# Optimization experiments

Measured on AMD Instinct MI355X. Metric: run time of the kernel, lower is better.

Reference implementation:

```python
import jax, jax.numpy as jnp
import numpy as np

D_MODEL = 1024
EXPAND = 2
D_INNER = EXPAND * D_MODEL          # 2048
D_STATE = 64
NGROUPS = 1
HEADDIM = 128
NHEADS = D_INNER // HEADDIM         # 16
D_CONV = 4
CONV_DIM = D_INNER + 2 * NGROUPS * D_STATE      # 2176
D_IN_PROJ = 2 * D_INNER + 2 * NGROUPS * D_STATE + NHEADS  # 4240
BATCH = 2
SEQLEN = 4096
RMS_EPS = 1e-5


def setup_inputs() -> dict:
    key = jax.random.key(0)
    ks = jax.random.split(key, 8)
    u = jax.random.normal(ks[0], (BATCH, SEQLEN, D_MODEL), jnp.float32)
    in_proj_w = jax.random.normal(ks[1], (D_IN_PROJ, D_MODEL), jnp.float32) * 0.02
    conv_w = jax.random.normal(ks[2], (CONV_DIM, D_CONV), jnp.float32) * 0.2
    conv_b = jax.random.normal(ks[3], (CONV_DIM,), jnp.float32) * 0.1
    dt_bias = jax.random.normal(ks[4], (NHEADS,), jnp.float32) * 0.5
    # A ~ Uniform(1,16), A_log = log(A)  (as in Mamba2 init)
    A_log = jnp.log(jax.random.uniform(ks[5], (NHEADS,), jnp.float32, 1.0, 16.0))
    D = jnp.ones((NHEADS,), jnp.float32)
    rms_w = jnp.ones((D_INNER,), jnp.float32)
    out_w = jax.random.normal(ks[6], (D_MODEL, D_INNER), jnp.float32) * 0.02
    return {"u": u, "in_proj_w": in_proj_w, "conv_w": conv_w, "conv_b": conv_b,
            "dt_bias": dt_bias, "A_log": A_log, "D": D, "rms_w": rms_w, "out_w": out_w}


def reference(u, in_proj_w, conv_w, conv_b, dt_bias, A_log, D, rms_w, out_w):
    Bsz, L, _ = u.shape
    # in_proj: (B,L,d_model) -> (B,L,d_in_proj), split [z, x, B, C, dt]
    zxbcdt = jnp.einsum('bld,ed->ble', u, in_proj_w)
    s1 = D_INNER
    s2 = 2 * D_INNER
    s3 = s2 + NGROUPS * D_STATE
    s4 = s3 + NGROUPS * D_STATE
    z = zxbcdt[..., :s1]
    x = zxbcdt[..., s1:s2]
    B_part = zxbcdt[..., s2:s3]
    C_part = zxbcdt[..., s3:s4]
    dt = zxbcdt[..., s4:]
    dt = jax.nn.softplus(dt + dt_bias)            # (B,L,H), dt_limit=(0,inf) -> no clamp

    # depthwise causal conv1d + silu over [x, B, C]
    xBC = jnp.concatenate([x, B_part, C_part], axis=-1)      # (B,L,CONV_DIM)
    xt = xBC.transpose(0, 2, 1)                              # (B,C,L)
    kern = conv_w[:, None, :]                                # (C,1,W)
    conv = jax.lax.conv_general_dilated(
        xt, kern, (1,), [(D_CONV - 1, 0)],
        dimension_numbers=('NCH', 'OIH', 'NCH'),
        feature_group_count=CONV_DIM)
    xBC = jax.nn.silu((conv + conv_b[None, :, None]).transpose(0, 2, 1))

    x_c = xBC[..., :D_INNER]
    B_c = xBC[..., D_INNER:D_INNER + NGROUPS * D_STATE]
    C_c = xBC[..., D_INNER + NGROUPS * D_STATE:]
    x_s = x_c.reshape(Bsz, L, NHEADS, HEADDIM)               # (B,L,H,P)
    hpg = NHEADS // NGROUPS
    B_full = jnp.repeat(B_c.reshape(Bsz, L, NGROUPS, D_STATE), hpg, axis=2)  # (B,L,H,N)
    C_full = jnp.repeat(C_c.reshape(Bsz, L, NGROUPS, D_STATE), hpg, axis=2)

    A = -jnp.exp(A_log)                                      # (H,)

    def step(state, inp):
        x_t, dt_t, B_t, C_t = inp  # (B,H,P),(B,H),(B,H,N),(B,H,N)
        decay = jnp.exp(dt_t * A)[:, :, None, None]          # (B,H,1,1)
        state = decay * state + B_t[:, :, None, :] * x_t[..., None]  # (B,H,P,N)
        y_t = jnp.einsum('bhpn,bhn->bhp', state, C_t)
        return state, y_t

    init = jnp.zeros((Bsz, NHEADS, HEADDIM, D_STATE), u.dtype)
    xs = (x_s.transpose(1, 0, 2, 3), dt.transpose(1, 0, 2),
          B_full.transpose(1, 0, 2, 3), C_full.transpose(1, 0, 2, 3))
    _, ys = jax.lax.scan(step, init, xs)                     # (L,B,H,P)
    y = ys.transpose(1, 0, 2, 3) + D[None, None, :, None] * x_s

    y_flat = y.reshape(Bsz, L, D_INNER)
    mu = jnp.mean(y_flat * y_flat, axis=-1, keepdims=True)
    y_flat = y_flat * jax.lax.rsqrt(mu + RMS_EPS) * rms_w    # RMSNorm
    y_flat = y_flat * jax.nn.sigmoid(z)                      # gate
    return jnp.einsum('bld,ed->ble', y_flat, out_w)          # out_proj (no bias)
```

## Files before the change

### kernel.cpp

```cpp
#include <hip/hip_runtime.h>
#include <math.h>

#define D_MODEL   1024
#define D_INNER   2048
#define D_STATE   64
#define HEADDIM   128
#define NHEADS    16
#define D_CONV    4
#define BATCH     2
#define SEQLEN    4096
#define RMS_EPS   1e-5f
#define D_IN_PROJ 4240

#define ZX_LD     4224

#define LCHUNK    128
#define NCHUNK    (SEQLEN / LCHUNK)

typedef __attribute__((ext_vector_type(8))) short short8;
typedef __attribute__((ext_vector_type(4))) float f32x4;

__device__ __forceinline__ ushort f2bf(float f) {
  unsigned u = __float_as_uint(f);
  u += 0x7fff + ((u >> 16) & 1);
  return (ushort)(u >> 16);
}
__device__ __forceinline__ float bf2f(ushort h) {
  return __uint_as_float(((unsigned)h) << 16);
}
__device__ __forceinline__ void ld4(const float* p, float* d) {
  float4 v = *(const float4*)p; d[0] = v.x; d[1] = v.y; d[2] = v.z; d[3] = v.w;
}
__device__ __forceinline__ void ld4b(const ushort* p, float* d) {
  ushort4 v = *(const ushort4*)p;
  d[0] = bf2f(v.x); d[1] = bf2f(v.y); d[2] = bf2f(v.z); d[3] = bf2f(v.w);
}

__device__ __forceinline__ void gl_lds16(const ushort* g, ushort* l) {
  __builtin_amdgcn_global_load_lds(
      (const __attribute__((address_space(1))) unsigned int*)g,
      (__attribute__((address_space(3))) unsigned int*)l, 16, 0, 0);
}

__global__ void cvt_split(const float* __restrict__ w,
                          ushort* __restrict__ hi, ushort* __restrict__ lo, int n4) {
  int i = blockIdx.x * 256 + threadIdx.x;
  if (i >= n4) return;
  float4 v = ((const float4*)w)[i];
  ushort h0 = f2bf(v.x), h1 = f2bf(v.y), h2 = f2bf(v.z), h3 = f2bf(v.w);
  ushort l0 = f2bf(v.x - bf2f(h0)), l1 = f2bf(v.y - bf2f(h1));
  ushort l2 = f2bf(v.z - bf2f(h2)), l3 = f2bf(v.w - bf2f(h3));
  ((ushort4*)hi)[i] = make_ushort4(h0, h1, h2, h3);
  ((ushort4*)lo)[i] = make_ushort4(l0, l1, l2, l3);
}

template<int BM, int BK, bool ALO, bool OBF16>
__launch_bounds__(256, 3)
__global__ void gemm_bf16p(const ushort* __restrict__ Ah, const ushort* __restrict__ Al,
                           const ushort* __restrict__ Bh, const ushort* __restrict__ Bl,
                           float* __restrict__ C, int ldc,
                           int M, int N, int ldab, int Kslice, int n1term) {
  constexpr int BN = 128;
  constexpr int NQ = BK / 8;
  constexpr int RT = BM / 32;
  constexpr int CT = 4;
  constexpr int KS = BK / 32;

  __shared__ ushort As[ALO ? 2 : 1][BM * BK];
  __shared__ ushort Bs[2][BN * BK];

  const int bn   = blockIdx.x * BN;
  if (bn >= N) return;
  const bool two = (bn >= n1term);
  const int t    = threadIdx.x;
  const int bm   = blockIdx.y * BM;
  const int kz   = blockIdx.z;
  const int kb   = kz * Kslice;
  C += (size_t)kz * M * ldc;
  const int wave = t >> 6, lane = t & 63;
  const int ml   = lane & 15, g4 = lane >> 4;
  const int sw   = ml & (NQ - 1);
  const int wr   = wave & 1, wc = wave >> 1;
  const int r0   = wr * RT * 16, c0 = wc * CT * 16;

  f32x4 acc[RT][CT];
#pragma unroll
  for (int i = 0; i < RT; ++i)
#pragma unroll
    for (int j = 0; j < CT; ++j) acc[i][j] = (f32x4){0.f, 0.f, 0.f, 0.f};

  for (int k0 = kb; k0 < kb + Kslice; k0 += BK) {
    __syncthreads();
#pragma unroll
    for (int ii = 0; ii < BM * NQ / 256; ++ii) {
      int idx = t + ii * 256;
      int row = idx / NQ, qs = idx % NQ;
      int qg  = qs ^ (row & (NQ - 1));
      size_t go = (size_t)(bm + row) * ldab + k0 + qg * 8;
      gl_lds16(Ah + go, &As[0][idx * 8]);
      if (ALO) gl_lds16(Al + go, &As[ALO ? 1 : 0][idx * 8]);
    }
#pragma unroll
    for (int ii = 0; ii < BN * NQ / 256; ++ii) {
      int idx = t + ii * 256;
      int row = idx / NQ, qs = idx % NQ;
      int qg  = qs ^ (row & (NQ - 1));
      size_t go = (size_t)(bn + row) * ldab + k0 + qg * 8;
      gl_lds16(Bh + go, &Bs[0][idx * 8]);
      if (two) gl_lds16(Bl + go, &Bs[1][idx * 8]);
    }
    __syncthreads();

#pragma unroll
    for (int ks = 0; ks < KS; ++ks) {
      const int qA = ((ks * 4 + g4) ^ sw) * 8;
      short8 ah[RT], al[RT], bh[CT], bl[CT];
#pragma unroll
      for (int i = 0; i < RT; ++i) {
        int off = (r0 + i * 16 + ml) * BK + qA;
        ah[i] = *(const short8*)&As[0][off];
        if (ALO) al[i] = *(const short8*)&As[ALO ? 1 : 0][off];
      }
#pragma unroll
      for (int j = 0; j < CT; ++j) {
        int off = (c0 + j * 16 + ml) * BK + qA;
        bh[j] = *(const short8*)&Bs[0][off];
        if (two) bl[j] = *(const short8*)&Bs[1][off];
      }
#pragma unroll
      for (int i = 0; i < RT; ++i)
#pragma unroll
        for (int j = 0; j < CT; ++j) {
          acc[i][j] = __builtin_amdgcn_mfma_f32_16x16x32_bf16(ah[i], bh[j], acc[i][j], 0, 0, 0);
          if (two)
            acc[i][j] = __builtin_amdgcn_mfma_f32_16x16x32_bf16(ah[i], bl[j], acc[i][j], 0, 0, 0);
          if (ALO)
            acc[i][j] = __builtin_amdgcn_mfma_f32_16x16x32_bf16(al[i], bh[j], acc[i][j], 0, 0, 0);
        }
    }
  }

#pragma unroll
  for (int i = 0; i < RT; ++i)
#pragma unroll
    for (int j = 0; j < CT; ++j) {
      int col = bn + c0 + j * 16 + ml;
      if (col < N) {
        int rowb = bm + r0 + i * 16 + g4 * 4;
#pragma unroll
        for (int r = 0; r < 4; ++r) {
          if (OBF16) ((ushort*)C)[(size_t)(rowb + r) * ldc + col] = f2bf(acc[i][j][r]);
          else       C[(size_t)(rowb + r) * ldc + col] = acc[i][j][r];
        }
      }
    }
}

__global__ void add_out(const float* __restrict__ P, float* __restrict__ out, int n4) {
  int i = blockIdx.x * 256 + threadIdx.x;
  if (i >= n4) return;
  float4 a = ((const float4*)P)[i];
  float4 b = ((const float4*)(P + (size_t)SEQLEN * D_MODEL))[i];
  ((float4*)out)[i] = make_float4(a.x + b.x, a.y + b.y, a.z + b.z, a.w + b.w);
}

__global__ void add_dt(const float* __restrict__ P, float* __restrict__ dtb) {
  int i = blockIdx.x * 256 + threadIdx.x;
  if (i >= SEQLEN * NHEADS / 4) return;
  float4 s = ((const float4*)P)[i];
#pragma unroll
  for (int k = 1; k < 8; ++k) {
    float4 v = ((const float4*)(P + (size_t)k * SEQLEN * NHEADS))[i];
    s.x += v.x; s.y += v.y; s.z += v.z; s.w += v.w;
  }
  ((float4*)dtb)[i] = s;
}


__device__ __forceinline__ void cum_scan(float* cum, float v, int t, float* carry) {
  int lane = t & 63;
#pragma unroll
  for (int off = 1; off < 64; off <<= 1) {
    float o = __shfl_up(v, off);
    if (lane >= off) v += o;
  }
  if (t == 63) *carry = v;
  __syncthreads();
  if (t >= 64 && t < LCHUNK) v += *carry;
  if (t < LCHUNK) cum[t] = v;
  __syncthreads();
}

__device__ __forceinline__ void conv4b(const ushort* __restrict__ zx,
                                       const float* __restrict__ cw,
                                       const float* __restrict__ cb,
                                       int l, int col0, float* outv) {
  const ushort* bp = zx + (size_t)l * ZX_LD + col0;
  float r3[4], r2[4], r1[4], r0[4], bb[4];
  ld4b(bp, r3);
  if (l >= 1) ld4b(bp - ZX_LD, r2);     else { r2[0]=r2[1]=r2[2]=r2[3]=0.f; }
  if (l >= 2) ld4b(bp - 2 * ZX_LD, r1); else { r1[0]=r1[1]=r1[2]=r1[3]=0.f; }
  if (l >= 3) ld4b(bp - 3 * ZX_LD, r0); else { r0[0]=r0[1]=r0[2]=r0[3]=0.f; }
  const int ch = col0 - 2048;
  ld4(cb + ch, bb);
#pragma unroll
  for (int j = 0; j < 4; ++j) {
    float w4[4]; ld4(cw + (ch + j) * 4, w4);
    float a = bb[j];
    a = fmaf(w4[0], r0[j], a);
    a = fmaf(w4[1], r1[j], a);
    a = fmaf(w4[2], r2[j], a);
    a = fmaf(w4[3], r3[j], a);
    outv[j] = a / (1.f + __expf(-a));
  }
}

__launch_bounds__(256, 2)
__global__ void passA_ssd(const ushort* __restrict__ zx,
                          const float* __restrict__ dtb,
                          const float* __restrict__ cw, const float* __restrict__ cb,
                          const float* __restrict__ dt_bias,
                          const float* __restrict__ A_log,
                          float* __restrict__ Sc, float* __restrict__ Pc) {
  const int blk = blockIdx.x;
  const int c   = blk & (NCHUNK - 1);
  const int h   = blk >> 5;
  const int l0  = c * LCHUNK;
  const int t   = threadIdx.x;
  const int wave = t >> 6, lane = t & 63;
  const int ml = lane & 15, g4 = lane >> 4;
  const float Ah = -expf(A_log[h]);

  __shared__ float cum[LCHUNK];
  __shared__ float carry;
  __shared__ ushort Xt[2][LCHUNK * 40];
  __shared__ ushort Bt[2][D_STATE * 40];

  {
    float v = 0.f;
    if (t < LCHUNK) {
      float xv = dtb[(size_t)(l0 + t) * NHEADS + h] + dt_bias[h];
      float sp = (xv > 20.f) ? xv : log1pf(expf(xv));
      v = sp * Ah;
    }
    cum_scan(cum, v, t, &carry);
  }
  const float cend = cum[LCHUNK - 1];

  f32x4 acc[2][4];
#pragma unroll
  for (int i = 0; i < 2; ++i)
#pragma unroll
    for (int j = 0; j < 4; ++j) acc[i][j] = (f32x4){0.f, 0.f, 0.f, 0.f};
  const int p0 = wave * 32;

  for (int slab = 0; slab < 4; ++slab) {
    __syncthreads();
    for (int i = 0; i < 4; ++i) {
      int q = t + i * 256;
      int s = q >> 5, p4 = (q & 31) * 4;
      int l = l0 + slab * 32 + s;
      float xv[4];
      conv4b(zx, cw, cb, l, 2048 + h * HEADDIM + p4, xv);
#pragma unroll
      for (int j = 0; j < 4; ++j) {
        ushort hh = f2bf(xv[j]);
        Xt[0][(p4 + j) * 40 + s] = hh;
        Xt[1][(p4 + j) * 40 + s] = f2bf(xv[j] - bf2f(hh));
      }
    }
    for (int i = 0; i < 2; ++i) {
      int q = t + i * 256;
      int s = q >> 4, n4 = (q & 15) * 4;
      int l = l0 + slab * 32 + s;
      float wd = __expf(cend - cum[slab * 32 + s]);
      float bv[4];
      conv4b(zx, cw, cb, l, 4096 + n4, bv);
#pragma unroll
      for (int j = 0; j < 4; ++j) {
        float val = bv[j] * wd;
        ushort hh = f2bf(val);
        Bt[0][(n4 + j) * 40 + s] = hh;
        Bt[1][(n4 + j) * 40 + s] = f2bf(val - bf2f(hh));
      }
    }
    __syncthreads();

    short8 xa_h[2], xa_l[2];
#pragma unroll
    for (int pi = 0; pi < 2; ++pi) {
      int off = (p0 + pi * 16 + ml) * 40 + g4 * 8;
      xa_h[pi] = *(const short8*)&Xt[0][off];
      xa_l[pi] = *(const short8*)&Xt[1][off];
    }
#pragma unroll
    for (int ni = 0; ni < 4; ++ni) {
      int off = (ni * 16 + ml) * 40 + g4 * 8;
      short8 bh = *(const short8*)&Bt[0][off];
      short8 bl = *(const short8*)&Bt[1][off];
#pragma unroll
      for (int pi = 0; pi < 2; ++pi) {
        acc[pi][ni] = __builtin_amdgcn_mfma_f32_16x16x32_bf16(xa_h[pi], bh, acc[pi][ni], 0, 0, 0);
        acc[pi][ni] = __builtin_amdgcn_mfma_f32_16x16x32_bf16(xa_h[pi], bl, acc[pi][ni], 0, 0, 0);
        acc[pi][ni] = __builtin_amdgcn_mfma_f32_16x16x32_bf16(xa_l[pi], bh, acc[pi][ni], 0, 0, 0);
      }
    }
  }

  float* S = Sc + (size_t)blk * (HEADDIM * D_STATE);
#pragma unroll
  for (int pi = 0; pi < 2; ++pi)
#pragma unroll
    for (int ni = 0; ni < 4; ++ni) {
      int n = ni * 16 + ml;
#pragma unroll
      for (int r = 0; r < 4; ++r) {
        int p = p0 + pi * 16 + g4 * 4 + r;
        S[(size_t)p * D_STATE + n] = acc[pi][ni][r];
      }
    }
  if (t == 0) Pc[blk] = __expf(cend);
}

__global__ void scan_passB(float* __restrict__ Sc, const float* __restrict__ Pc) {
  const int h = blockIdx.x;
  const int e = blockIdx.y * 512 + threadIdx.x;
  const size_t hb = (size_t)h * NCHUNK;
  float st = 0.f;
  for (int c = 0; c < NCHUNK; ++c) {
    size_t idx = (hb + c) * (HEADDIM * D_STATE) + e;
    float P = Pc[hb + c];
    float v = Sc[idx];
    Sc[idx] = st;
    st = fmaf(P, st, v);
  }
}

__launch_bounds__(256, 2)
__global__ void passC_ssd(const ushort* __restrict__ zx,
                          const float* __restrict__ dtb,
                          const float* __restrict__ cw, const float* __restrict__ cb,
                          const float* __restrict__ dt_bias,
                          const float* __restrict__ A_log,
                          const float* __restrict__ Dp,
                          const float* __restrict__ Sc,
                          float* __restrict__ ybuf) {
  const int blk = blockIdx.x;
  const int c   = blk & (NCHUNK - 1);
  const int h   = blk >> 5;
  const int l0  = c * LCHUNK;
  const int t   = threadIdx.x;
  const int wave = t >> 6, lane = t & 63;
  const int ml = lane & 15, g4 = lane >> 4;
  const float Ah = -expf(A_log[h]);
  const float Dh = Dp[h];

  __shared__ float cum[LCHUNK];
  __shared__ float carry;
  __shared__ ushort Csl[2][2][LCHUNK * 32];
  __shared__ ushort Bsl[2][2][32 * 32];
  __shared__ ushort Msl[2][LCHUNK * 32];
  __shared__ ushort Xt[2][LCHUNK * 40];

  {
    float v = 0.f;
    if (t < LCHUNK) {
      float xv = dtb[(size_t)(l0 + t) * NHEADS + h] + dt_bias[h];
      float sp = (xv > 20.f) ? xv : log1pf(expf(xv));
      v = sp * Ah;
    }
    cum_scan(cum, v, t, &carry);
  }

  {
    int row = t >> 1, half = t & 1;
    int l = l0 + row;
    int colbase = 4160 + half * 32;
#pragma unroll
    for (int j0 = 0; j0 < 32; j0 += 4) {
      float cv[4];
      conv4b(zx, cw, cb, l, colbase + j0, cv);
      ushort h0 = f2bf(cv[0]), h1 = f2bf(cv[1]), h2 = f2bf(cv[2]), h3 = f2bf(cv[3]);
      *(ushort4*)&Csl[half][0][row * 32 + j0] = make_ushort4(h0, h1, h2, h3);
      *(ushort4*)&Csl[half][1][row * 32 + j0] =
          make_ushort4(f2bf(cv[0] - bf2f(h0)), f2bf(cv[1] - bf2f(h1)),
                       f2bf(cv[2] - bf2f(h2)), f2bf(cv[3] - bf2f(h3)));
    }
  }

  f32x4 accY[2][8];
#pragma unroll
  for (int i = 0; i < 2; ++i)
#pragma unroll
    for (int j = 0; j < 8; ++j) accY[i][j] = (f32x4){0.f, 0.f, 0.f, 0.f};
  const int t0 = wave * 32;

  for (int slab = 0; slab < 4; ++slab) {
    __syncthreads();
    for (int i = 0; i < 2; ++i) {
      int q = t + i * 256;
      int s = q >> 4, c4 = (q & 15) * 4;
      int l = l0 + slab * 32 + s;
      float bv[4];
      conv4b(zx, cw, cb, l, 4096 + c4, bv);
      int ks = c4 >> 5, jj = c4 & 31;
      ushort h0 = f2bf(bv[0]), h1 = f2bf(bv[1]), h2 = f2bf(bv[2]), h3 = f2bf(bv[3]);
      *(ushort4*)&Bsl[ks][0][s * 32 + jj] = make_ushort4(h0, h1, h2, h3);
      *(ushort4*)&Bsl[ks][1][s * 32 + jj] =
          make_ushort4(f2bf(bv[0] - bf2f(h0)), f2bf(bv[1] - bf2f(h1)),
                       f2bf(bv[2] - bf2f(h2)), f2bf(bv[3] - bf2f(h3)));
    }
    for (int i = 0; i < 4; ++i) {
      int q = t + i * 256;
      int s = q >> 5, p4 = (q & 31) * 4;
      int l = l0 + slab * 32 + s;
      float xv[4];
      conv4b(zx, cw, cb, l, 2048 + h * HEADDIM + p4, xv);
#pragma unroll
      for (int j = 0; j < 4; ++j) {
        ushort hh = f2bf(xv[j]);
        Xt[0][(p4 + j) * 40 + s] = hh;
        Xt[1][(p4 + j) * 40 + s] = f2bf(xv[j] - bf2f(hh));
      }
    }
    __syncthreads();

    f32x4 g[2][2];
#pragma unroll
    for (int i = 0; i < 2; ++i)
#pragma unroll
      for (int j = 0; j < 2; ++j) g[i][j] = (f32x4){0.f, 0.f, 0.f, 0.f};
#pragma unroll
    for (int ks = 0; ks < 2; ++ks) {
      short8 ca_h[2], ca_l[2];
#pragma unroll
      for (int ti = 0; ti < 2; ++ti) {
        int off = (t0 + ti * 16 + ml) * 32 + g4 * 8;
        ca_h[ti] = *(const short8*)&Csl[ks][0][off];
        ca_l[ti] = *(const short8*)&Csl[ks][1][off];
      }
#pragma unroll
      for (int si = 0; si < 2; ++si) {
        int off = (si * 16 + ml) * 32 + g4 * 8;
        short8 bh = *(const short8*)&Bsl[ks][0][off];
        short8 bl = *(const short8*)&Bsl[ks][1][off];
#pragma unroll
        for (int ti = 0; ti < 2; ++ti) {
          g[ti][si] = __builtin_amdgcn_mfma_f32_16x16x32_bf16(ca_h[ti], bh, g[ti][si], 0, 0, 0);
          g[ti][si] = __builtin_amdgcn_mfma_f32_16x16x32_bf16(ca_h[ti], bl, g[ti][si], 0, 0, 0);
          g[ti][si] = __builtin_amdgcn_mfma_f32_16x16x32_bf16(ca_l[ti], bh, g[ti][si], 0, 0, 0);
        }
      }
    }
#pragma unroll
    for (int ti = 0; ti < 2; ++ti)
#pragma unroll
      for (int si = 0; si < 2; ++si) {
        int sl = si * 16 + ml;
        int sg = slab * 32 + sl;
#pragma unroll
        for (int r = 0; r < 4; ++r) {
          int tg = t0 + ti * 16 + g4 * 4 + r;
          float coeff = (sg <= tg) ? __expf(cum[tg] - cum[sg]) : 0.f;
          float val = g[ti][si][r] * coeff + ((sg == tg) ? Dh : 0.f);
          ushort hh = f2bf(val);
          Msl[0][tg * 32 + sl] = hh;
          Msl[1][tg * 32 + sl] = f2bf(val - bf2f(hh));
        }
      }
    __syncthreads();
    {
      short8 ma_h[2], ma_l[2];
#pragma unroll
      for (int ti = 0; ti < 2; ++ti) {
        int off = (t0 + ti * 16 + ml) * 32 + g4 * 8;
        ma_h[ti] = *(const short8*)&Msl[0][off];
        ma_l[ti] = *(const short8*)&Msl[1][off];
      }
#pragma unroll
      for (int pi = 0; pi < 8; ++pi) {
        int off = (pi * 16 + ml) * 40 + g4 * 8;
        short8 xh = *(const short8*)&Xt[0][off];
        short8 xl = *(const short8*)&Xt[1][off];
#pragma unroll
        for (int ti = 0; ti < 2; ++ti) {
          accY[ti][pi] = __builtin_amdgcn_mfma_f32_16x16x32_bf16(ma_h[ti], xh, accY[ti][pi], 0, 0, 0);
          accY[ti][pi] = __builtin_amdgcn_mfma_f32_16x16x32_bf16(ma_h[ti], xl, accY[ti][pi], 0, 0, 0);
          accY[ti][pi] = __builtin_amdgcn_mfma_f32_16x16x32_bf16(ma_l[ti], xh, accY[ti][pi], 0, 0, 0);
        }
      }
    }
  }

  const float* S = Sc + (size_t)blk * (HEADDIM * D_STATE);
  for (int ns = 0; ns < 2; ++ns) {
    __syncthreads();
    for (int i = 0; i < 4; ++i) {
      int q = t + i * 256;
      int p = q >> 3, j4 = (q & 7) * 4;
      float4 v = *(const float4*)(S + (size_t)p * D_STATE + ns * 32 + j4);
      float vv[4] = {v.x, v.y, v.z, v.w};
      ushort hh0 = f2bf(vv[0]), hh1 = f2bf(vv[1]), hh2 = f2bf(vv[2]), hh3 = f2bf(vv[3]);
      *(ushort4*)&Xt[0][p * 40 + j4] = make_ushort4(hh0, hh1, hh2, hh3);
      *(ushort4*)&Xt[1][p * 40 + j4] =
          make_ushort4(f2bf(vv[0] - bf2f(hh0)), f2bf(vv[1] - bf2f(hh1)),
                       f2bf(vv[2] - bf2f(hh2)), f2bf(vv[3] - bf2f(hh3)));
    }
    {
      int row = t >> 1, j0 = (t & 1) * 16;
      float e = __expf(cum[row]);
#pragma unroll
      for (int j = 0; j < 16; ++j) {
        int idx = row * 32 + j0 + j;
        float cv = bf2f(Csl[ns][0][idx]) + bf2f(Csl[ns][1][idx]);
        float val = cv * e;
        ushort hh = f2bf(val);
        Msl[0][idx] = hh;
        Msl[1][idx] = f2bf(val - bf2f(hh));
      }
    }
    __syncthreads();
    {
      short8 ma_h[2], ma_l[2];
#pragma unroll
      for (int ti = 0; ti < 2; ++ti) {
        int off = (t0 + ti * 16 + ml) * 32 + g4 * 8;
        ma_h[ti] = *(const short8*)&Msl[0][off];
        ma_l[ti] = *(const short8*)&Msl[1][off];
      }
#pragma unroll
      for (int pi = 0; pi < 8; ++pi) {
        int off = (pi * 16 + ml) * 40 + g4 * 8;
        short8 xh = *(const short8*)&Xt[0][off];
        short8 xl = *(const short8*)&Xt[1][off];
#pragma unroll
        for (int ti = 0; ti < 2; ++ti) {
          accY[ti][pi] = __builtin_amdgcn_mfma_f32_16x16x32_bf16(ma_h[ti], xh, accY[ti][pi], 0, 0, 0);
          accY[ti][pi] = __builtin_amdgcn_mfma_f32_16x16x32_bf16(ma_h[ti], xl, accY[ti][pi], 0, 0, 0);
          accY[ti][pi] = __builtin_amdgcn_mfma_f32_16x16x32_bf16(ma_l[ti], xh, accY[ti][pi], 0, 0, 0);
        }
      }
    }
  }

#pragma unroll
  for (int ti = 0; ti < 2; ++ti)
#pragma unroll
    for (int pi = 0; pi < 8; ++pi) {
      int p = pi * 16 + ml;
#pragma unroll
      for (int r = 0; r < 4; ++r) {
        int l = l0 + t0 + ti * 16 + g4 * 4 + r;
        ybuf[(size_t)l * D_INNER + h * HEADDIM + p] = accY[ti][pi][r];
      }
    }
}

__launch_bounds__(256)
__global__ void rmsnorm_gate_split(const float* __restrict__ ybuf,
                                   const ushort* __restrict__ zx,
                                   const float* __restrict__ rms_w,
                                   ushort* __restrict__ yh) {
  const int row = blockIdx.x;
  const int t   = threadIdx.x;
  const float* y  = ybuf + (size_t)row * D_INNER;
  const ushort* z = zx   + (size_t)row * ZX_LD;

  float4 a  = *(const float4*)(y + t * 8);
  float4 bq = *(const float4*)(y + t * 8 + 4);
  float ss = a.x * a.x + a.y * a.y + a.z * a.z + a.w * a.w +
             bq.x * bq.x + bq.y * bq.y + bq.z * bq.z + bq.w * bq.w;
#pragma unroll
  for (int off = 32; off > 0; off >>= 1) ss += __shfl_down(ss, off);
  __shared__ float red[4];
  if ((t & 63) == 0) red[t >> 6] = ss;
  __syncthreads();
  float tot = red[0] + red[1] + red[2] + red[3];
  float scale = rsqrtf(tot * (1.f / (float)D_INNER) + RMS_EPS);

  float vy[8] = {a.x, a.y, a.z, a.w, bq.x, bq.y, bq.z, bq.w};
  ushort4 zv0 = *(const ushort4*)(z + t * 8);
  ushort4 zv1 = *(const ushort4*)(z + t * 8 + 4);
  ushort zz[8] = {zv0.x, zv0.y, zv0.z, zv0.w, zv1.x, zv1.y, zv1.z, zv1.w};
  ushort hh[8];
#pragma unroll
  for (int jj = 0; jj < 8; ++jj) {
    int col = t * 8 + jj;
    float g = 1.f / (1.f + __expf(-bf2f(zz[jj])));
    float v = vy[jj] * scale * rms_w[col] * g;
    hh[jj] = f2bf(v);
  }
  size_t o = (size_t)row * D_INNER + t * 8;
  *(ushort4*)(yh + o)     = make_ushort4(hh[0], hh[1], hh[2], hh[3]);
  *(ushort4*)(yh + o + 4) = make_ushort4(hh[4], hh[5], hh[6], hh[7]);
}

extern "C" void kernel_launch(void* const* d_in, const int* in_sizes, int n_in,
                              void* d_out, int out_size, void* d_ws, size_t ws_size,
                              hipStream_t stream) {
  const float* u         = (const float*)d_in[0];
  const float* in_proj_w = (const float*)d_in[1];
  const float* conv_w    = (const float*)d_in[2];
  const float* conv_b    = (const float*)d_in[3];
  const float* dt_bias   = (const float*)d_in[4];
  const float* A_log     = (const float*)d_in[5];
  const float* Dp        = (const float*)d_in[6];
  const float* rms_w     = (const float*)d_in[7];
  const float* out_w     = (const float*)d_in[8];
  float* out = (float*)d_out;

  float* ws    = (float*)d_ws;
  ushort* zxbc = (ushort*)ws;
  float* dtb   = ws   + (size_t)SEQLEN * ZX_LD / 2;
  float* dtp   = dtb  + (size_t)SEQLEN * NHEADS;
  float* ybuf  = dtp  + (size_t)8 * SEQLEN * NHEADS;
  float* Pc    = ybuf + (size_t)SEQLEN * D_INNER;
  float* Sc    = Pc   + 512;
  ushort* uh   = (ushort*)(Sc + (size_t)NHEADS * NCHUNK * HEADDIM * D_STATE);
  ushort* ul   = uh  + (size_t)SEQLEN * D_MODEL;
  ushort* w1h  = ul  + (size_t)SEQLEN * D_MODEL;
  ushort* w1l  = w1h + (size_t)D_IN_PROJ * D_MODEL;
  ushort* w2h  = w1l + (size_t)D_IN_PROJ * D_MODEL;
  ushort* w2l  = w2h + (size_t)D_MODEL * D_INNER;
  ushort* yh   = (ushort*)Sc;
  float* Opart = ybuf;

  {
    int n4 = D_IN_PROJ * D_MODEL / 4;
    cvt_split<<<(n4 + 255) / 256, 256, 0, stream>>>(in_proj_w, w1h, w1l, n4);
    int m4 = D_MODEL * D_INNER / 4;
    cvt_split<<<(m4 + 255) / 256, 256, 0, stream>>>(out_w, w2h, w2l, m4);
  }

  for (int b = 0; b < BATCH; ++b) {
    const float* u_b  = u   + (size_t)b * SEQLEN * D_MODEL;
    float*      out_b = out + (size_t)b * SEQLEN * D_MODEL;

    {
      int n4 = SEQLEN * D_MODEL / 4;
      cvt_split<<<(n4 + 255) / 256, 256, 0, stream>>>(u_b, uh, ul, n4);
    }

    {
      dim3 g(40, SEQLEN / 128, 1);
      gemm_bf16p<128, 64, false, true><<<g, 256, 0, stream>>>(uh, uh, w1h, w1l,
                                                          (float*)zxbc, ZX_LD, SEQLEN,
                                                          ZX_LD, D_MODEL, D_MODEL,
                                                          D_INNER);
    }
    {
      const ushort* bh = w1h + (size_t)ZX_LD * D_MODEL;
      const ushort* bl = w1l + (size_t)ZX_LD * D_MODEL;
      dim3 g(1, SEQLEN / 128, 8);
      gemm_bf16p<128, 32, true, false><<<g, 256, 0, stream>>>(uh, ul, bh, bl,
                                                          dtp, NHEADS, SEQLEN, NHEADS,
                                                          D_MODEL, D_MODEL / 8, 0);
      add_dt<<<(SEQLEN * NHEADS / 4 + 255) / 256, 256, 0, stream>>>(dtp, dtb);
    }

    passA_ssd<<<NHEADS * NCHUNK, 256, 0, stream>>>(zxbc, dtb, conv_w, conv_b,
                                                   dt_bias, A_log, Sc, Pc);
    scan_passB<<<dim3(NHEADS, (HEADDIM * D_STATE) / 512), 512, 0, stream>>>(Sc, Pc);
    passC_ssd<<<NHEADS * NCHUNK, 256, 0, stream>>>(zxbc, dtb, conv_w, conv_b,
                                                   dt_bias, A_log, Dp, Sc, ybuf);

    rmsnorm_gate_split<<<SEQLEN, 256, 0, stream>>>(ybuf, zxbc, rms_w, yh);

    {
      dim3 g(D_MODEL / 128, SEQLEN / 128, 2);
      gemm_bf16p<128, 64, false, false><<<g, 256, 0, stream>>>(yh, yh, w2h, w2l,
                                                           Opart, D_MODEL, SEQLEN, D_MODEL,
                                                           D_INNER, D_INNER / 2, 0);
    }
    add_out<<<(SEQLEN * D_MODEL / 4 + 255) / 256, 256, 0, stream>>>(Opart, out_b,
                                                                    SEQLEN * D_MODEL / 4);
  }
}
```

Before: 555.9 us.

## Reuse passA conv outputs in passC, skip masked causal tiles, keep C in registers

passA now writes the convolved x and B values to global scratch buffers (reusing ybuf and dtp), so passC reads them instead of recomputing the depthwise conv and SiLU. passC loads the C fragments into registers once, through a swizzled shared layout, instead of re-reading them every slab. Waves whose query rows lie entirely before the current key slab skip the causally masked C·B and M·X MFMA work. A block barrier is replaced by a wave-local LDS wait, since each wave only touches its own Msl rows. The cost is extra global writes in passA and the loss of conv-recompute independence between the passes.

```diff
diff --git a/kernel.cpp b/kernel.cpp
--- a/kernel.cpp
+++ b/kernel.cpp
@@ -221,7 +221,8 @@
                           const float* __restrict__ cw, const float* __restrict__ cb,
                           const float* __restrict__ dt_bias,
                           const float* __restrict__ A_log,
-                          float* __restrict__ Sc, float* __restrict__ Pc) {
+                          float* __restrict__ Sc, float* __restrict__ Pc,
+                          float* __restrict__ xconv, float* __restrict__ bconv) {
   const int blk = blockIdx.x;
   const int c   = blk & (NCHUNK - 1);
   const int h   = blk >> 5;
@@ -262,6 +263,8 @@
       int l = l0 + slab * 32 + s;
       float xv[4];
       conv4b(zx, cw, cb, l, 2048 + h * HEADDIM + p4, xv);
+      *(float4*)(xconv + (size_t)l * D_INNER + h * HEADDIM + p4) =
+          make_float4(xv[0], xv[1], xv[2], xv[3]);
 #pragma unroll
       for (int j = 0; j < 4; ++j) {
         ushort hh = f2bf(xv[j]);
@@ -276,6 +279,9 @@
       float wd = __expf(cend - cum[slab * 32 + s]);
       float bv[4];
       conv4b(zx, cw, cb, l, 4096 + n4, bv);
+      if (h == 0)
+        *(float4*)(bconv + (size_t)l * D_STATE + n4) =
+            make_float4(bv[0], bv[1], bv[2], bv[3]);
 #pragma unroll
       for (int j = 0; j < 4; ++j) {
         float val = bv[j] * wd;
@@ -344,6 +350,7 @@
                           const float* __restrict__ A_log,
                           const float* __restrict__ Dp,
                           const float* __restrict__ Sc,
+                          const float* __restrict__ bconv,
                           float* __restrict__ ybuf) {
   const int blk = blockIdx.x;
   const int c   = blk & (NCHUNK - 1);
@@ -352,14 +359,14 @@
   const int t   = threadIdx.x;
   const int wave = t >> 6, lane = t & 63;
   const int ml = lane & 15, g4 = lane >> 4;
+  const int t0 = wave * 32;
   const float Ah = -expf(A_log[h]);
   const float Dh = Dp[h];
 
   __shared__ float cum[LCHUNK];
   __shared__ float carry;
-  __shared__ ushort Csl[2][2][LCHUNK * 32];
-  __shared__ ushort Bsl[2][2][32 * 32];
-  __shared__ ushort Msl[2][LCHUNK * 32];
+  __shared__ ushort Bsl[2][2][32 * 40];
+  __shared__ ushort Msl[2][LCHUNK * 40];
   __shared__ ushort Xt[2][LCHUNK * 40];
 
   {
@@ -372,7 +379,10 @@
     cum_scan(cum, v, t, &carry);
   }
 
+  short8 c_h[2][2], c_l[2][2];
   {
+    ushort* CSh = &Msl[0][0];
+    ushort* CSl = &Xt[0][0];
     int row = t >> 1, half = t & 1;
     int l = l0 + row;
     int colbase = 4160 + half * 32;
@@ -380,12 +390,25 @@
     for (int j0 = 0; j0 < 32; j0 += 4) {
       float cv[4];
       conv4b(zx, cw, cb, l, colbase + j0, cv);
+      int colc = half * 32 + j0;
+      int quad = colc >> 3;
+      int addr = row * 64 + ((quad ^ (row & 7)) << 3) + (colc & 7);
       ushort h0 = f2bf(cv[0]), h1 = f2bf(cv[1]), h2 = f2bf(cv[2]), h3 = f2bf(cv[3]);
-      *(ushort4*)&Csl[half][0][row * 32 + j0] = make_ushort4(h0, h1, h2, h3);
-      *(ushort4*)&Csl[half][1][row * 32 + j0] =
-          make_ushort4(f2bf(cv[0] - bf2f(h0)), f2bf(cv[1] - bf2f(h1)),
-                       f2bf(cv[2] - bf2f(h2)), f2bf(cv[3] - bf2f(h3)));
-    }
+      *(ushort4*)&CSh[addr] = make_ushort4(h0, h1, h2, h3);
+      *(ushort4*)&CSl[addr] = make_ushort4(
+          f2bf(cv[0] - bf2f(h0)), f2bf(cv[1] - bf2f(h1)),
+          f2bf(cv[2] - bf2f(h2)), f2bf(cv[3] - bf2f(h3)));
+    }
+    __syncthreads();
+#pragma unroll
+    for (int ks = 0; ks < 2; ++ks)
+#pragma unroll
+      for (int ti = 0; ti < 2; ++ti) {
+        int rw = t0 + ti * 16 + ml;
+        int ad = rw * 64 + (((ks * 4 + g4) ^ (rw & 7)) << 3);
+        c_h[ks][ti] = *(const short8*)&CSh[ad];
+        c_l[ks][ti] = *(const short8*)&CSl[ad];
+      }
   }
 
   f32x4 accY[2][8];
@@ -393,87 +416,84 @@
   for (int i = 0; i < 2; ++i)
 #pragma unroll
     for (int j = 0; j < 8; ++j) accY[i][j] = (f32x4){0.f, 0.f, 0.f, 0.f};
-  const int t0 = wave * 32;
+
+  const float* xcv = ybuf;
 
   for (int slab = 0; slab < 4; ++slab) {
     __syncthreads();
+#pragma unroll
     for (int i = 0; i < 2; ++i) {
       int q = t + i * 256;
-      int s = q >> 4, c4 = (q & 15) * 4;
+      int s = q >> 4, n4 = (q & 15) * 4;
       int l = l0 + slab * 32 + s;
-      float bv[4];
-      conv4b(zx, cw, cb, l, 4096 + c4, bv);
-      int ks = c4 >> 5, jj = c4 & 31;
+      float4 v = *(const float4*)(bconv + (size_t)l * D_STATE + n4);
+      float bv[4] = {v.x, v.y, v.z, v.w};
+      int ks = n4 >> 5, jj = n4 & 31;
       ushort h0 = f2bf(bv[0]), h1 = f2bf(bv[1]), h2 = f2bf(bv[2]), h3 = f2bf(bv[3]);
-      *(ushort4*)&Bsl[ks][0][s * 32 + jj] = make_ushort4(h0, h1, h2, h3);
-      *(ushort4*)&Bsl[ks][1][s * 32 + jj] =
-          make_ushort4(f2bf(bv[0] - bf2f(h0)), f2bf(bv[1] - bf2f(h1)),
-                       f2bf(bv[2] - bf2f(h2)), f2bf(bv[3] - bf2f(h3)));
-    }
+      *(ushort4*)&Bsl[ks][0][s * 40 + jj] = make_ushort4(h0, h1, h2, h3);
+      *(ushort4*)&Bsl[ks][1][s * 40 + jj] = make_ushort4(
+          f2bf(bv[0] - bf2f(h0)), f2bf(bv[1] - bf2f(h1)),
+          f2bf(bv[2] - bf2f(h2)), f2bf(bv[3] - bf2f(h3)));
+    }
+#pragma unroll
     for (int i = 0; i < 4; ++i) {
       int q = t + i * 256;
-      int s = q >> 5, p4 = (q & 31) * 4;
-      int l = l0 + slab * 32 + s;
-      float xv[4];
-      conv4b(zx, cw, cb, l, 2048 + h * HEADDIM + p4, xv);
+      int p = q & 127, sg = q >> 7;
+      ushort hh[4], ll[4];
 #pragma unroll
       for (int j = 0; j < 4; ++j) {
-        ushort hh = f2bf(xv[j]);
-        Xt[0][(p4 + j) * 40 + s] = hh;
-        Xt[1][(p4 + j) * 40 + s] = f2bf(xv[j] - bf2f(hh));
-      }
-    }
-    __syncthreads();
-
-    f32x4 g[2][2];
-#pragma unroll
-    for (int i = 0; i < 2; ++i)
-#pragma unroll
-      for (int j = 0; j < 2; ++j) g[i][j] = (f32x4){0.f, 0.f, 0.f, 0.f};
-#pragma unroll
-    for (int ks = 0; ks < 2; ++ks) {
-      short8 ca_h[2], ca_l[2];
+        int l = l0 + slab * 32 + sg * 4 + j;
+        float xv = xcv[(size_t)l * D_INNER + h * HEADDIM + p];
+        hh[j] = f2bf(xv);
+        ll[j] = f2bf(xv - bf2f(hh[j]));
+      }
+      *(ushort4*)&Xt[0][p * 40 + sg * 4] = make_ushort4(hh[0], hh[1], hh[2], hh[3]);
+      *(ushort4*)&Xt[1][p * 40 + sg * 4] = make_ushort4(ll[0], ll[1], ll[2], ll[3]);
+    }
+    __syncthreads();
+
+    if (wave >= slab) {
+      f32x4 g[2][2];
+#pragma unroll
+      for (int i = 0; i < 2; ++i)
+#pragma unroll
+        for (int j = 0; j < 2; ++j) g[i][j] = (f32x4){0.f, 0.f, 0.f, 0.f};
+#pragma unroll
+      for (int ks = 0; ks < 2; ++ks) {
+#pragma unroll
+        for (int si = 0; si < 2; ++si) {
+          int off = (si * 16 + ml) * 40 + g4 * 8;
+          short8 bh = *(const short8*)&Bsl[ks][0][off];
+          short8 bl = *(const short8*)&Bsl[ks][1][off];
+#pragma unroll
+          for (int ti = 0; ti < 2; ++ti) {
+            g[ti][si] = __builtin_amdgcn_mfma_f32_16x16x32_bf16(c_h[ks][ti], bh, g[ti][si], 0, 0, 0);
+            g[ti][si] = __builtin_amdgcn_mfma_f32_16x16x32_bf16(c_h[ks][ti], bl, g[ti][si], 0, 0, 0);
+            g[ti][si] = __builtin_amdgcn_mfma_f32_16x16x32_bf16(c_l[ks][ti], bh, g[ti][si], 0, 0, 0);
+          }
+        }
+      }
+#pragma unroll
+      for (int ti = 0; ti < 2; ++ti)
+#pragma unroll
+        for (int si = 0; si < 2; ++si) {
+          int sl = si * 16 + ml;
+          int sg = slab * 32 + sl;
+#pragma unroll
+          for (int r = 0; r < 4; ++r) {
+            int tg = t0 + ti * 16 + g4 * 4 + r;
+            float coeff = (sg <= tg) ? __expf(cum[tg] - cum[sg]) : 0.f;
+            float val = g[ti][si][r] * coeff + ((sg == tg) ? Dh : 0.f);
+            ushort hh = f2bf(val);
+            Msl[0][tg * 40 + sl] = hh;
+            Msl[1][tg * 40 + sl] = f2bf(val - bf2f(hh));
+          }
+        }
+      asm volatile("s_waitcnt lgkmcnt(0)" ::: "memory");
+      short8 ma_h[2], ma_l[2];
 #pragma unroll
       for (int ti = 0; ti < 2; ++ti) {
-        int off = (t0 + ti * 16 + ml) * 32 + g4 * 8;
-        ca_h[ti] = *(const short8*)&Csl[ks][0][off];
-        ca_l[ti] = *(const short8*)&Csl[ks][1][off];
-      }
-#pragma unroll
-      for (int si = 0; si < 2; ++si) {
-        int off = (si * 16 + ml) * 32 + g4 * 8;
-        short8 bh = *(const short8*)&Bsl[ks][0][off];
-        short8 bl = *(const short8*)&Bsl[ks][1][off];
-#pragma unroll
-        for (int ti = 0; ti < 2; ++ti) {
-          g[ti][si] = __builtin_amdgcn_mfma_f32_16x16x32_bf16(ca_h[ti], bh, g[ti][si], 0, 0, 0);
-          g[ti][si] = __builtin_amdgcn_mfma_f32_16x16x32_bf16(ca_h[ti], bl, g[ti][si], 0, 0, 0);
-          g[ti][si] = __builtin_amdgcn_mfma_f32_16x16x32_bf16(ca_l[ti], bh, g[ti][si], 0, 0, 0);
-        }
-      }
-    }
-#pragma unroll
-    for (int ti = 0; ti < 2; ++ti)
-#pragma unroll
-      for (int si = 0; si < 2; ++si) {
-        int sl = si * 16 + ml;
-        int sg = slab * 32 + sl;
-#pragma unroll
-        for (int r = 0; r < 4; ++r) {
-          int tg = t0 + ti * 16 + g4 * 4 + r;
-          float coeff = (sg <= tg) ? __expf(cum[tg] - cum[sg]) : 0.f;
-          float val = g[ti][si][r] * coeff + ((sg == tg) ? Dh : 0.f);
-          ushort hh = f2bf(val);
-          Msl[0][tg * 32 + sl] = hh;
-          Msl[1][tg * 32 + sl] = f2bf(val - bf2f(hh));
-        }
-      }
-    __syncthreads();
-    {
-      short8 ma_h[2], ma_l[2];
-#pragma unroll
-      for (int ti = 0; ti < 2; ++ti) {
-        int off = (t0 + ti * 16 + ml) * 32 + g4 * 8;
+        int off = (t0 + ti * 16 + ml) * 40 + g4 * 8;
         ma_h[ti] = *(const short8*)&Msl[0][off];
         ma_l[ti] = *(const short8*)&Msl[1][off];
       }
@@ -493,8 +513,10 @@
   }
 
   const float* S = Sc + (size_t)blk * (HEADDIM * D_STATE);
+#pragma unroll
   for (int ns = 0; ns < 2; ++ns) {
     __syncthreads();
+#pragma unroll
     for (int i = 0; i < 4; ++i) {
       int q = t + i * 256;
       int p = q >> 3, j4 = (q & 7) * 4;
@@ -506,39 +528,29 @@
           make_ushort4(f2bf(vv[0] - bf2f(hh0)), f2bf(vv[1] - bf2f(hh1)),
                        f2bf(vv[2] - bf2f(hh2)), f2bf(vv[3] - bf2f(hh3)));
     }
-    {
-      int row = t >> 1, j0 = (t & 1) * 16;
-      float e = __expf(cum[row]);
-#pragma unroll
-      for (int j = 0; j < 16; ++j) {
-        int idx = row * 32 + j0 + j;
-        float cv = bf2f(Csl[ns][0][idx]) + bf2f(Csl[ns][1][idx]);
-        float val = cv * e;
-        ushort hh = f2bf(val);
-        Msl[0][idx] = hh;
-        Msl[1][idx] = f2bf(val - bf2f(hh));
-      }
-    }
-    __syncthreads();
-    {
-      short8 ma_h[2], ma_l[2];
+    __syncthreads();
+    short8 ma_h[2], ma_l[2];
+#pragma unroll
+    for (int ti = 0; ti < 2; ++ti) {
+      float e = __expf(cum[t0 + ti * 16 + ml]);
+#pragma unroll
+      for (int j = 0; j < 8; ++j) {
+        float v = (bf2f((ushort)c_h[ns][ti][j]) + bf2f((ushort)c_l[ns][ti][j])) * e;
+        ushort hh = f2bf(v);
+        ma_h[ti][j] = (short)hh;
+        ma_l[ti][j] = (short)f2bf(v - bf2f(hh));
+      }
+    }
+#pragma unroll
+    for (int pi = 0; pi < 8; ++pi) {
+      int off = (pi * 16 + ml) * 40 + g4 * 8;
+      short8 xh = *(const short8*)&Xt[0][off];
+      short8 xl = *(const short8*)&Xt[1][off];
 #pragma unroll
       for (int ti = 0; ti < 2; ++ti) {
-        int off = (t0 + ti * 16 + ml) * 32 + g4 * 8;
-        ma_h[ti] = *(const short8*)&Msl[0][off];
-        ma_l[ti] = *(const short8*)&Msl[1][off];
-      }
-#pragma unroll
-      for (int pi = 0; pi < 8; ++pi) {
-        int off = (pi * 16 + ml) * 40 + g4 * 8;
-        short8 xh = *(const short8*)&Xt[0][off];
-        short8 xl = *(const short8*)&Xt[1][off];
-#pragma unroll
-        for (int ti = 0; ti < 2; ++ti) {
-          accY[ti][pi] = __builtin_amdgcn_mfma_f32_16x16x32_bf16(ma_h[ti], xh, accY[ti][pi], 0, 0, 0);
-          accY[ti][pi] = __builtin_amdgcn_mfma_f32_16x16x32_bf16(ma_h[ti], xl, accY[ti][pi], 0, 0, 0);
-          accY[ti][pi] = __builtin_amdgcn_mfma_f32_16x16x32_bf16(ma_l[ti], xh, accY[ti][pi], 0, 0, 0);
-        }
+        accY[ti][pi] = __builtin_amdgcn_mfma_f32_16x16x32_bf16(ma_h[ti], xh, accY[ti][pi], 0, 0, 0);
+        accY[ti][pi] = __builtin_amdgcn_mfma_f32_16x16x32_bf16(ma_h[ti], xl, accY[ti][pi], 0, 0, 0);
+        accY[ti][pi] = __builtin_amdgcn_mfma_f32_16x16x32_bf16(ma_l[ti], xh, accY[ti][pi], 0, 0, 0);
       }
     }
   }
@@ -624,6 +636,7 @@
   ushort* w2l  = w2h + (size_t)D_MODEL * D_INNER;
   ushort* yh   = (ushort*)Sc;
   float* Opart = ybuf;
+  float* bconv = dtp;
 
   {
     int n4 = D_IN_PROJ * D_MODEL / 4;
@@ -659,10 +672,12 @@
     }
 
     passA_ssd<<<NHEADS * NCHUNK, 256, 0, stream>>>(zxbc, dtb, conv_w, conv_b,
-                                                   dt_bias, A_log, Sc, Pc);
+                                                   dt_bias, A_log, Sc, Pc,
+                                                   ybuf, bconv);
     scan_passB<<<dim3(NHEADS, (HEADDIM * D_STATE) / 512), 512, 0, stream>>>(Sc, Pc);
     passC_ssd<<<NHEADS * NCHUNK, 256, 0, stream>>>(zxbc, dtb, conv_w, conv_b,
-                                                   dt_bias, A_log, Dp, Sc, ybuf);
+                                                   dt_bias, A_log, Dp, Sc,
+                                                   bconv, ybuf);
 
     rmsnorm_gate_split<<<SEQLEN, 256, 0, stream>>>(ybuf, zxbc, rms_w, yh);
 
```

Result: faster. 536.8 us (-3.4%).
